# Performance work log

Measured on AMD Instinct MI355X. Metric: run time of the kernel, lower is better.

The kernel has to match this reference:

```python
import jax, jax.numpy as jnp
import numpy as np

T = 1.0
N_NEG = 50
NUM_CLASSES = 500  # smoothing denominator K from CrossEntropyLabelSmooth (faithful quirk)
EPS = 0.1

B, C, D = 2048, 65536, 256


def setup_inputs() -> dict:
    key = jax.random.key(0)
    k1, k2, k3 = jax.random.split(key, 3)
    f = jax.random.normal(k1, (B, D), dtype=jnp.float32)
    centers = jax.random.normal(k2, (C, D), dtype=jnp.float32)
    label = jax.random.randint(k3, (B,), 0, C, dtype=jnp.int64)
    return {"f": f, "centers": centers, "label": label}


def reference(f, centers, label):
    b = f.shape[0]
    rows = jnp.arange(b)
    mat = f @ centers.T                              # [B, C] similarity scores
    pos = mat[rows, label][:, None]                  # [B, 1] positive score
    # mask the positive column so top-k picks only negatives
    masked = mat.at[rows, label].set(-jnp.inf)
    neg, _ = jax.lax.top_k(masked, N_NEG)            # [B, N_neg]
    preds = jnp.concatenate([pos, neg], axis=1) / T  # [B, 1 + N_neg]
    log_probs = jax.nn.log_softmax(preds, axis=1)
    # label-smoothed one-hot with target class 0 (the positive)
    onehot = jnp.zeros_like(log_probs).at[:, 0].set(1.0)
    targets = (1.0 - EPS) * onehot + EPS / NUM_CLASSES
    loss = (-targets * log_probs).mean(0).sum()
    return loss
```

## Files before the change

### kernel.cpp

```cpp
#include <hip/hip_runtime.h>
#include <hip/hip_fp16.h>

#define B_ROWS 2048
#define C_COLS 65536
#define D_DIM  256
#define N_NEG  50
#define NTILES (C_COLS / 128)
#define SN 136

typedef __attribute__((ext_vector_type(8))) short short8;
typedef __attribute__((ext_vector_type(4))) float floatx4;
typedef __fp16 f16x2 __attribute__((ext_vector_type(2)));
typedef __fp16 h8v  __attribute__((ext_vector_type(8)));
typedef __fp16 h4v  __attribute__((ext_vector_type(4)));
typedef __fp16 h2v  __attribute__((ext_vector_type(2)));

__device__ __forceinline__ ushort f2bf(float f) {
  unsigned u = __float_as_uint(f);
  unsigned r = (u + 0x7FFFu + ((u >> 16) & 1u)) >> 16;
  return (ushort)r;
}

__global__ void cvt_swz(const float* __restrict__ in, ushort* __restrict__ out, int n8) {
  int i = blockIdx.x * blockDim.x + threadIdx.x;
  if (i >= n8) return;
  int row = i >> 5;
  int ka  = i & 31;
  int ktile = ka >> 3, kb = ka & 7;
  const float4* src = (const float4*)(in + (size_t)i * 8);
  float4 a = src[0], b = src[1];
  ushort4 o0, o1;
  o0.x = f2bf(a.x); o0.y = f2bf(a.y); o0.z = f2bf(a.z); o0.w = f2bf(a.w);
  o1.x = f2bf(b.x); o1.y = f2bf(b.y); o1.z = f2bf(b.z); o1.w = f2bf(b.w);
  ushort* dst = out + (size_t)row * D_DIM + ktile * 64 + ((kb ^ (row & 7)) << 3);
  ((ushort4*)dst)[0] = o0;
  ((ushort4*)dst)[1] = o1;
}

__device__ __forceinline__ void async16(const void* g, void* l) {
  __builtin_amdgcn_global_load_lds((const __attribute__((address_space(1))) void*)g,
                                   (__attribute__((address_space(3))) void*)l,
                                   16, 0, 0);
}

template <bool PREB>
__global__ void gemm_reduce(const ushort* __restrict__ fb,
                            const ushort* __restrict__ cb,
                            const float* __restrict__ cen,
                            const int* __restrict__ label,
                            float* __restrict__ cand) {
  __shared__ __align__(16) char smem[SN * 128 * 2];
  __shared__ int labLDS[128];
  ushort* Cs = (ushort*)smem;
  ushort* Fs = Cs + 8192;
  ushort* scu = (ushort*)smem;

  const int tid = threadIdx.x, wave = tid >> 6, lane = tid & 63;
  const int l = lane & 15, q = lane >> 4;
  const int m0 = blockIdx.x * 128, n0 = blockIdx.y * 128;
  const int bxTile = blockIdx.y;
  if (tid < 128) labLDS[tid] = label[m0 + tid];

  floatx4 acc[4][4] = {};
  const int wn = (wave >> 1) * 64, wm = (wave & 1) * 64;

  for (int kt = 0; kt < D_DIM / 64; ++kt) {
#pragma unroll
    for (int r = 0; r < 4; ++r) {
      int idx = r * 2048 + wave * 512 + lane * 8;
      int row = idx >> 6, kk = idx & 63;
      async16(fb + (size_t)(m0 + row) * D_DIM + kt * 64 + kk, Fs + r * 2048 + wave * 512);
      if (PREB)
        async16(cb + (size_t)(n0 + row) * D_DIM + kt * 64 + kk, Cs + r * 2048 + wave * 512);
    }
    if (!PREB) {
#pragma unroll
      for (int g = 0; g < 4; ++g) {
        int e = (tid + g * 256) * 8;
        int row = e >> 6, kblk = (e >> 3) & 7;
        const float* gp = cen + (size_t)(n0 + row) * D_DIM + kt * 64 + kblk * 8;
        float4 fa = *(const float4*)gp;
        float4 fbv = *(const float4*)(gp + 4);
        uint4 o;
        o.x = (uint)f2bf(fa.x)  | ((uint)f2bf(fa.y)  << 16);
        o.y = (uint)f2bf(fa.z)  | ((uint)f2bf(fa.w)  << 16);
        o.z = (uint)f2bf(fbv.x) | ((uint)f2bf(fbv.y) << 16);
        o.w = (uint)f2bf(fbv.z) | ((uint)f2bf(fbv.w) << 16);
        *(uint4*)(Cs + (row << 6) + ((kblk ^ (row & 7)) << 3)) = o;
      }
    }
    __syncthreads();

#pragma unroll
    for (int ks = 0; ks < 2; ++ks) {
      short8 a[4], b[4];
#pragma unroll
      for (int i = 0; i < 4; ++i) {
        int swz = ((4 * ks + q) ^ (l & 7)) << 3;
        a[i] = *(const short8*)(Cs + ((wn + i * 16 + l) << 6) + swz);
        b[i] = *(const short8*)(Fs + ((wm + i * 16 + l) << 6) + swz);
      }
#pragma unroll
      for (int i = 0; i < 4; ++i)
#pragma unroll
        for (int j = 0; j < 4; ++j)
          acc[i][j] = __builtin_amdgcn_mfma_f32_16x16x32_bf16(a[i], b[j], acc[i][j], 0, 0, 0);
    }
    __syncthreads();
  }

  __half* sc = (__half*)scu;
#pragma unroll
  for (int i = 0; i < 4; ++i)
#pragma unroll
    for (int j = 0; j < 4; ++j) {
      int mloc = wm + j * 16 + l;
      int nloc = wn + i * 16 + q * 4;
      f16x2 h0 = __builtin_amdgcn_cvt_pkrtz(acc[i][j][0], acc[i][j][1]);
      f16x2 h1 = __builtin_amdgcn_cvt_pkrtz(acc[i][j][2], acc[i][j][3]);
      uint2 w;
      w.x = *(const uint*)&h0;
      w.y = *(const uint*)&h1;
      *(uint2*)(sc + mloc * SN + nloc) = w;
    }
  __syncthreads();

  {
    const int r = tid >> 1, hf = tid & 1;
    const ushort* bp = scu + r * SN + hf * 64;
    const int rel = labLDS[r] - (n0 + hf * 64);
    if ((unsigned)rel < 64u) ((ushort*)bp)[rel] = 0xFC00;
    float outv[4];
#pragma unroll
    for (int g = 0; g < 4; ++g) {
      h8v v0 = ((const h8v*)bp)[g * 2];
      h8v v1 = ((const h8v*)bp)[g * 2 + 1];
      h8v m8 = __builtin_elementwise_max(v0, v1);
      h4v m4 = __builtin_elementwise_max(m8.lo, m8.hi);
      h2v m2 = __builtin_elementwise_max(m4.lo, m4.hi);
      outv[g] = fmaxf((float)m2.x, (float)m2.y);
    }
    *(float4*)(cand + ((size_t)(m0 + r) * NTILES + bxTile) * 8 + hf * 4) =
        make_float4(outv[0], outv[1], outv[2], outv[3]);
  }
}

__device__ __forceinline__ float dec_key(int k) {
  if (k < 0x0400) return -INFINITY;
  ushort h = (k >= 0x8000) ? (ushort)(k ^ 0x8000) : (ushort)(~k & 0xFFFF);
  __half_raw hr; hr.x = h;
  return __half2float((__half)hr);
}

__global__ void final_select(const float* __restrict__ cand, const float* __restrict__ f,
                             const float* __restrict__ cen, const int* __restrict__ label,
                             float* __restrict__ rowloss) {
  __shared__ float sred[8];
  __shared__ int   sint[8];
  const int row = blockIdx.x, tid = threadIdx.x;
  const int lane = tid & 63, wid = tid >> 6;
  const int lab = label[row];

  float v[16];
  const float4* p = (const float4*)(cand + (size_t)row * (NTILES * 8));
#pragma unroll
  for (int g = 0; g < 4; ++g) {
    float4 u = p[tid + g * 256];
    v[g * 4 + 0] = u.x; v[g * 4 + 1] = u.y; v[g * 4 + 2] = u.z; v[g * 4 + 3] = u.w;
  }
  float pv = f[(size_t)row * D_DIM + tid] * cen[(size_t)lab * D_DIM + tid];
  float m = -INFINITY;
#pragma unroll
  for (int k = 0; k < 16; ++k) m = fmaxf(m, v[k]);
#pragma unroll
  for (int o = 32; o > 0; o >>= 1) {
    m = fmaxf(m, __shfl_down(m, o));
    pv += __shfl_down(pv, o);
  }
  if (lane == 0) { sred[wid] = m; sred[4 + wid] = pv; }
  __syncthreads();
  m = fmaxf(fmaxf(sred[0], sred[1]), fmaxf(sred[2], sred[3]));
  const float pos = sred[4] + sred[5] + sred[6] + sred[7];

  __half hm = __float2half(m);
  int hb = (int)(*(ushort*)&hm);
  int km = (m >= 0.f) ? (0x8000 | hb) : (~hb & 0xFFFF);
  int lo = km - 2048, hi = km;
  if (lo < 0x0400) lo = 0x0400;
#pragma unroll
  for (int it = 0; it < 12; ++it) {
    int mid = (lo + hi) >> 1;
    float tau = dec_key(mid);
    int c = 0;
#pragma unroll
    for (int k = 0; k < 16; ++k) c += (v[k] > tau) ? 1 : 0;
#pragma unroll
    for (int o = 32; o > 0; o >>= 1) c += __shfl_down(c, o);
    if (lane == 0) sint[(it & 1) * 4 + wid] = c;
    __syncthreads();
    int base = (it & 1) * 4;
    int tot = sint[base] + sint[base + 1] + sint[base + 2] + sint[base + 3];
    if (tot <= 49) hi = mid; else lo = mid + 1;
  }

  const float tau = dec_key(hi);
  float sum = 0.f, se = 0.f; int c = 0;
#pragma unroll
  for (int k = 0; k < 16; ++k) {
    if (v[k] > tau) { ++c; sum += v[k]; se += expf(v[k] - m); }
  }
#pragma unroll
  for (int o = 32; o > 0; o >>= 1) {
    sum += __shfl_down(sum, o);
    se  += __shfl_down(se, o);
    c   += __shfl_down(c, o);
  }
  if (lane == 0) { sred[wid] = sum; sred[4 + wid] = se; sint[wid] = c; }
  __syncthreads();
  if (tid == 0) {
    float S = sred[0] + sred[1] + sred[2] + sred[3];
    float E = sred[4] + sred[5] + sred[6] + sred[7];
    int   C = sint[0] + sint[1] + sint[2] + sint[3];
    float nfill = (float)(N_NEG - C);
    S += nfill * tau;
    E += nfill * expf(tau - m);
    float M = fmaxf(m, pos);
    float seAll = E * expf(m - M) + expf(pos - M);
    float lse = M + logf(seAll);
    rowloss[row] = 0.9102f * lse - 0.9002f * pos - 2.0e-4f * S;
  }
}

__global__ void sum_loss(const float* __restrict__ rowloss, float* __restrict__ out) {
  __shared__ float red[4];
  const int tid = threadIdx.x;
  float s = 0.f;
  for (int i = tid; i < B_ROWS; i += 256) s += rowloss[i];
#pragma unroll
  for (int o = 32; o > 0; o >>= 1) s += __shfl_down(s, o);
  if ((tid & 63) == 0) red[tid >> 6] = s;
  __syncthreads();
  if (tid == 0) out[0] = (red[0] + red[1] + red[2] + red[3]) * (1.0f / B_ROWS);
}

extern "C" void kernel_launch(void* const* d_in, const int* in_sizes, int n_in,
                              void* d_out, int out_size, void* d_ws, size_t ws_size,
                              hipStream_t stream) {
  const float* f   = (const float*)d_in[0];
  const float* cen = (const float*)d_in[1];
  const int*   label = (const int*)d_in[2];
  float* out = (float*)d_out;

  char* ws = (char*)d_ws;
  float*  cand    = (float*)ws;
  ushort* fb      = (ushort*)(ws + 33554432);
  float*  rowloss = (float*)(ws + 34611200);
  ushort* cb      = (ushort*)(ws + 34619392);
  const bool pre = ws_size >= (34619392ull + 33554432ull);

  cvt_swz<<<256, 256, 0, stream>>>(f, fb, (B_ROWS * D_DIM) / 8);

  dim3 grid(B_ROWS / 128, NTILES);
  if (pre) {
    cvt_swz<<<8192, 256, 0, stream>>>(cen, cb, (C_COLS * D_DIM) / 8);
    gemm_reduce<true><<<grid, 256, 0, stream>>>(fb, cb, cen, label, cand);
  } else {
    gemm_reduce<false><<<grid, 256, 0, stream>>>(fb, nullptr, cen, label, cand);
  }

  final_select<<<B_ROWS, 256, 0, stream>>>(cand, f, cen, label, rowloss);
  sum_loss<<<1, 256, 0, stream>>>(rowloss, out);
}
```

Measured before the change: 199.3 us.

## Use 32x32 MFMA and reduce group maxima in registers instead of LDS

Switches the GEMM inner loop from 16x16x32 to 32x32x16 bf16 MFMA with a 2x2 accumulator grid per wave. The epilogue now masks the label column and computes the per-16-column maxima straight from the accumulator registers, combining the two half-waves with a cross-lane shuffle. This removes the fp16 round trip through LDS and one block barrier, and keeps the maxima in fp32. It also merges the two bf16 conversion kernels into one launch and adds launch bounds to target 4 blocks per CU, which could raise register pressure or cause spills.

```diff
diff --git a/kernel.cpp b/kernel.cpp
--- a/kernel.cpp
+++ b/kernel.cpp
@@ -6,14 +6,9 @@
 #define D_DIM  256
 #define N_NEG  50
 #define NTILES (C_COLS / 128)
-#define SN 136
 
 typedef __attribute__((ext_vector_type(8))) short short8;
-typedef __attribute__((ext_vector_type(4))) float floatx4;
-typedef __fp16 f16x2 __attribute__((ext_vector_type(2)));
-typedef __fp16 h8v  __attribute__((ext_vector_type(8)));
-typedef __fp16 h4v  __attribute__((ext_vector_type(4)));
-typedef __fp16 h2v  __attribute__((ext_vector_type(2)));
+typedef __attribute__((ext_vector_type(16))) float floatx16;
 
 __device__ __forceinline__ ushort f2bf(float f) {
   unsigned u = __float_as_uint(f);
@@ -21,20 +16,22 @@
   return (ushort)r;
 }
 
-__global__ void cvt_swz(const float* __restrict__ in, ushort* __restrict__ out, int n8) {
+__global__ void cvt_both(const float* __restrict__ f, const float* __restrict__ cen,
+                         ushort* __restrict__ fb, ushort* __restrict__ cb, int doCen) {
   int i = blockIdx.x * blockDim.x + threadIdx.x;
-  if (i >= n8) return;
   int row = i >> 5;
-  int ka  = i & 31;
-  int ktile = ka >> 3, kb = ka & 7;
-  const float4* src = (const float4*)(in + (size_t)i * 8);
-  float4 a = src[0], b = src[1];
+  int ka = i & 31, ktile = ka >> 3, kb = ka & 7;
+  const float* src; ushort* dst; int r;
+  if (row < B_ROWS) { src = f; dst = fb; r = row; }
+  else { if (!doCen) return; src = cen; dst = cb; r = row - B_ROWS; }
+  const float4* s = (const float4*)(src + (size_t)r * D_DIM + ka * 8);
+  float4 a = s[0], b = s[1];
   ushort4 o0, o1;
   o0.x = f2bf(a.x); o0.y = f2bf(a.y); o0.z = f2bf(a.z); o0.w = f2bf(a.w);
   o1.x = f2bf(b.x); o1.y = f2bf(b.y); o1.z = f2bf(b.z); o1.w = f2bf(b.w);
-  ushort* dst = out + (size_t)row * D_DIM + ktile * 64 + ((kb ^ (row & 7)) << 3);
-  ((ushort4*)dst)[0] = o0;
-  ((ushort4*)dst)[1] = o1;
+  ushort* d = dst + (size_t)r * D_DIM + ktile * 64 + ((kb ^ (r & 7)) << 3);
+  ((ushort4*)d)[0] = o0;
+  ((ushort4*)d)[1] = o1;
 }
 
 __device__ __forceinline__ void async16(const void* g, void* l) {
@@ -44,24 +41,23 @@
 }
 
 template <bool PREB>
-__global__ void gemm_reduce(const ushort* __restrict__ fb,
-                            const ushort* __restrict__ cb,
-                            const float* __restrict__ cen,
-                            const int* __restrict__ label,
-                            float* __restrict__ cand) {
-  __shared__ __align__(16) char smem[SN * 128 * 2];
+__global__ __launch_bounds__(256, 4)
+void gemm_reduce(const ushort* __restrict__ fb,
+                 const ushort* __restrict__ cb,
+                 const float* __restrict__ cen,
+                 const int* __restrict__ label,
+                 float* __restrict__ cand) {
+  __shared__ __align__(16) ushort Cs[128 * 64];
+  __shared__ __align__(16) ushort Fs[128 * 64];
   __shared__ int labLDS[128];
-  ushort* Cs = (ushort*)smem;
-  ushort* Fs = Cs + 8192;
-  ushort* scu = (ushort*)smem;
 
   const int tid = threadIdx.x, wave = tid >> 6, lane = tid & 63;
-  const int l = lane & 15, q = lane >> 4;
+  const int ml = lane & 31, h = lane >> 5;
   const int m0 = blockIdx.x * 128, n0 = blockIdx.y * 128;
   const int bxTile = blockIdx.y;
   if (tid < 128) labLDS[tid] = label[m0 + tid];
 
-  floatx4 acc[4][4] = {};
+  floatx16 acc[2][2] = {};
   const int wn = (wave >> 1) * 64, wm = (wave & 1) * 64;
 
   for (int kt = 0; kt < D_DIM / 64; ++kt) {
@@ -92,56 +88,48 @@
     __syncthreads();
 
 #pragma unroll
-    for (int ks = 0; ks < 2; ++ks) {
-      short8 a[4], b[4];
-#pragma unroll
-      for (int i = 0; i < 4; ++i) {
-        int swz = ((4 * ks + q) ^ (l & 7)) << 3;
-        a[i] = *(const short8*)(Cs + ((wn + i * 16 + l) << 6) + swz);
-        b[i] = *(const short8*)(Fs + ((wm + i * 16 + l) << 6) + swz);
+    for (int ks = 0; ks < 4; ++ks) {
+      const int swz = ((2 * ks + h) ^ (ml & 7)) << 3;
+      short8 a[2], b[2];
+#pragma unroll
+      for (int i = 0; i < 2; ++i) {
+        a[i] = *(const short8*)(Cs + ((wn + i * 32 + ml) << 6) + swz);
+        b[i] = *(const short8*)(Fs + ((wm + i * 32 + ml) << 6) + swz);
       }
-#pragma unroll
-      for (int i = 0; i < 4; ++i)
-#pragma unroll
-        for (int j = 0; j < 4; ++j)
-          acc[i][j] = __builtin_amdgcn_mfma_f32_16x16x32_bf16(a[i], b[j], acc[i][j], 0, 0, 0);
+      acc[0][0] = __builtin_amdgcn_mfma_f32_32x32x16_bf16(a[0], b[0], acc[0][0], 0, 0, 0);
+      acc[0][1] = __builtin_amdgcn_mfma_f32_32x32x16_bf16(a[0], b[1], acc[0][1], 0, 0, 0);
+      acc[1][0] = __builtin_amdgcn_mfma_f32_32x32x16_bf16(a[1], b[0], acc[1][0], 0, 0, 0);
+      acc[1][1] = __builtin_amdgcn_mfma_f32_32x32x16_bf16(a[1], b[1], acc[1][1], 0, 0, 0);
     }
     __syncthreads();
   }
 
-  __half* sc = (__half*)scu;
-#pragma unroll
-  for (int i = 0; i < 4; ++i)
-#pragma unroll
-    for (int j = 0; j < 4; ++j) {
-      int mloc = wm + j * 16 + l;
-      int nloc = wn + i * 16 + q * 4;
-      f16x2 h0 = __builtin_amdgcn_cvt_pkrtz(acc[i][j][0], acc[i][j][1]);
-      f16x2 h1 = __builtin_amdgcn_cvt_pkrtz(acc[i][j][2], acc[i][j][3]);
-      uint2 w;
-      w.x = *(const uint*)&h0;
-      w.y = *(const uint*)&h1;
-      *(uint2*)(sc + mloc * SN + nloc) = w;
-    }
-  __syncthreads();
-
+  float gm[2][4];
+#pragma unroll
+  for (int j = 0; j < 2; ++j) {
+    const int lab = labLDS[wm + j * 32 + ml];
+#pragma unroll
+    for (int i = 0; i < 2; ++i) {
+      int rel = lab - (n0 + wn + i * 32);
+      if ((unsigned)rel < 32u && (((rel >> 2) & 1) == h)) {
+        int r4 = rel & ~4;
+        int reg = (r4 & 3) | ((r4 >> 3) << 2);
+        acc[i][j][reg] = -INFINITY;
+      }
+      float g0 = fmaxf(fmaxf(fmaxf(acc[i][j][0], acc[i][j][1]), fmaxf(acc[i][j][2], acc[i][j][3])),
+                       fmaxf(fmaxf(acc[i][j][4], acc[i][j][5]), fmaxf(acc[i][j][6], acc[i][j][7])));
+      float g1 = fmaxf(fmaxf(fmaxf(acc[i][j][8], acc[i][j][9]), fmaxf(acc[i][j][10], acc[i][j][11])),
+                       fmaxf(fmaxf(acc[i][j][12], acc[i][j][13]), fmaxf(acc[i][j][14], acc[i][j][15])));
+      g0 = fmaxf(g0, __shfl_xor(g0, 32));
+      g1 = fmaxf(g1, __shfl_xor(g1, 32));
+      gm[j][2 * i] = g0; gm[j][2 * i + 1] = g1;
+    }
+  }
   {
-    const int r = tid >> 1, hf = tid & 1;
-    const ushort* bp = scu + r * SN + hf * 64;
-    const int rel = labLDS[r] - (n0 + hf * 64);
-    if ((unsigned)rel < 64u) ((ushort*)bp)[rel] = 0xFC00;
-    float outv[4];
-#pragma unroll
-    for (int g = 0; g < 4; ++g) {
-      h8v v0 = ((const h8v*)bp)[g * 2];
-      h8v v1 = ((const h8v*)bp)[g * 2 + 1];
-      h8v m8 = __builtin_elementwise_max(v0, v1);
-      h4v m4 = __builtin_elementwise_max(m8.lo, m8.hi);
-      h2v m2 = __builtin_elementwise_max(m4.lo, m4.hi);
-      outv[g] = fmaxf((float)m2.x, (float)m2.y);
-    }
-    *(float4*)(cand + ((size_t)(m0 + r) * NTILES + bxTile) * 8 + hf * 4) =
-        make_float4(outv[0], outv[1], outv[2], outv[3]);
+    const int j = h;
+    float4 o = make_float4(gm[j][0], gm[j][1], gm[j][2], gm[j][3]);
+    int m = m0 + wm + j * 32 + ml;
+    *(float4*)(cand + (size_t)m * (NTILES * 8) + bxTile * 8 + (wn >> 4)) = o;
   }
 }
 
@@ -258,11 +246,10 @@
   ushort* cb      = (ushort*)(ws + 34619392);
   const bool pre = ws_size >= (34619392ull + 33554432ull);
 
-  cvt_swz<<<256, 256, 0, stream>>>(f, fb, (B_ROWS * D_DIM) / 8);
+  cvt_both<<<(B_ROWS + C_COLS) / 8, 256, 0, stream>>>(f, cen, fb, cb, pre ? 1 : 0);
 
   dim3 grid(B_ROWS / 128, NTILES);
   if (pre) {
-    cvt_swz<<<8192, 256, 0, stream>>>(cen, cb, (C_COLS * D_DIM) / 8);
     gemm_reduce<true><<<grid, 256, 0, stream>>>(fb, cb, cen, label, cand);
   } else {
     gemm_reduce<false><<<grid, 256, 0, stream>>>(fb, nullptr, cen, label, cand);
```

New measurement: 205.0 us. 1.03x slower.
